# Kernel optimization log

Measured on AMD Instinct MI355X. Metric: run time of the kernel, lower is better.

The kernel has to match this reference:

```python
import jax, jax.numpy as jnp
import numpy as np

NUM_CLASSES = 10
GAMMA = 1.0
EPS = 1e-12


def setup_inputs() -> dict:
    key = jax.random.key(0)
    k1, k2, k3, k4 = jax.random.split(key, 4)
    x = jax.random.normal(k1, (1024, 64), dtype=jnp.float32)
    exemplars = jax.random.normal(k2, (50000, 64), dtype=jnp.float32)
    exemplar_labels = jax.random.randint(k3, (50000,), 0, NUM_CLASSES)
    # beta_raw initialized as softplus^{-1}(init_beta) with init_beta=1.0
    init_beta = 1.0
    beta_raw = jnp.array([np.log(np.exp(init_beta) - 1.0)], dtype=jnp.float32)
    return {"x": x, "exemplars": exemplars, "exemplar_labels": exemplar_labels,
            "beta_raw": beta_raw}


def reference(x, exemplars, exemplar_labels, beta_raw):
    # Squared Euclidean distances (weight_diag == ones) via GEMM expansion:
    # d2[b, e] = ||x_b||^2 + ||e_e||^2 - 2 <x_b, e_e>
    x2 = jnp.sum(x * x, axis=-1, keepdims=True)            # (B, 1)
    e2 = jnp.sum(exemplars * exemplars, axis=-1)           # (Ne,)
    d2 = x2 + e2[None, :] - 2.0 * (x @ exemplars.T)        # (B, Ne)
    d2 = jnp.maximum(d2, 0.0)  # true sq-dist is nonneg; guards GEMM round-off
    beta = jax.nn.softplus(beta_raw[0])
    sims = jnp.exp(-beta * d2)                              # (B, Ne)
    # scatter-add similarities into per-class bins: (C, B) -> (B, C)
    class_sims = jax.ops.segment_sum(sims.T, exemplar_labels,
                                     num_segments=NUM_CLASSES).T
    logits = GAMMA * jnp.log(class_sims + EPS)
    return logits
```

## Files before the change

kernel.cpp:

```cpp
#include <hip/hip_runtime.h>


#define NB      1024
#define NE      50000
#define NE_PAD  50176
#define KD      64
#define NC      10
#define SROWS   64
#define NSTAGE  8
#define LROW    72

using half8   = __attribute__((ext_vector_type(8))) _Float16;
using half4v  = __attribute__((ext_vector_type(4))) _Float16;
using floatx4 = __attribute__((ext_vector_type(4))) float;

__device__ __forceinline__ float softplus_f(float x) {
  return (x > 20.f) ? x : log1pf(__expf(x));
}

__global__ __launch_bounds__(256) void prep_kernel(
    const float* __restrict__ x, const float* __restrict__ ex,
    const int* __restrict__ labels, const float* __restrict__ beta_raw,
    _Float16* __restrict__ ex_h, float* __restrict__ ce,
    _Float16* __restrict__ x_h, float* __restrict__ cb,
    float* __restrict__ class_sims, int* __restrict__ lab_pad)
{
  const int tid = threadIdx.x;
  const int gid = blockIdx.x * 256 + tid;
  if (gid < NB * NC) class_sims[gid] = 0.f;

  const float beta = softplus_f(beta_raw[0]);

  const int row = blockIdx.x * 16 + (tid >> 4);
  const int l16 = tid & 15;

  if (row < NE_PAD) {
    float4 v = make_float4(0.f, 0.f, 0.f, 0.f);
    if (row < NE) v = ((const float4*)ex)[row * 16 + l16];
    half4v hv = { (_Float16)v.x, (_Float16)v.y, (_Float16)v.z, (_Float16)v.w };
    *(half4v*)(ex_h + (size_t)row * KD + l16 * 4) = hv;
    float s = v.x*v.x + v.y*v.y + v.z*v.z + v.w*v.w;
    #pragma unroll
    for (int m = 1; m < 16; m <<= 1) s += __shfl_xor(s, m, 64);
    if (l16 == 0) ce[row] = (row < NE) ? (-beta * s) : -1e30f;
    if (l16 == 1) lab_pad[row] = (row < NE) ? labels[row] : 0;
  } else {
    const int rx = row - NE_PAD;
    float4 v = ((const float4*)x)[rx * 16 + l16];
    half4v hv = { (_Float16)v.x, (_Float16)v.y, (_Float16)v.z, (_Float16)v.w };
    *(half4v*)(x_h + (size_t)rx * KD + l16 * 4) = hv;
    float s = v.x*v.x + v.y*v.y + v.z*v.z + v.w*v.w;
    #pragma unroll
    for (int m = 1; m < 16; m <<= 1) s += __shfl_xor(s, m, 64);
    if (l16 == 0) cb[rx] = -beta * s;
  }
}

__global__ __launch_bounds__(256) void main_kernel(
    const _Float16* __restrict__ ex_h, const float* __restrict__ ce,
    const _Float16* __restrict__ x_h, const float* __restrict__ cb,
    const int* __restrict__ lab_pad, const float* __restrict__ beta_raw,
    float* __restrict__ class_sims)
{
  __shared__ _Float16 Ah[2][SROWS * LROW];
  __shared__ float    Ce[2][SROWS];
  __shared__ int      Lb[2][SROWS];

  const int tid  = threadIdx.x;
  const int wave = tid >> 6;
  const int lane = tid & 63;
  const int l15  = lane & 15;
  const int quad = lane >> 4;

  const int btile = blockIdx.x;
  const int chunk = blockIdx.y;
  const int e0    = chunk * 512;
  const int bm    = btile * 64 + wave * 16;

  const float beta = softplus_f(beta_raw[0]);
  const float s2 = 2.f * beta;

  const half8* xrow = (const half8*)(x_h + (size_t)(bm + l15) * KD);
  const half8 bx0 = xrow[quad];
  const half8 bx1 = xrow[quad + 4];
  const float cbl = cb[bm + l15];

  const int srow = tid >> 2;
  const int scol = tid & 3;
  const _Float16* gsrc = ex_h + (size_t)(e0 + srow) * KD + scol * 16;
  const int lofs = srow * LROW + scol * 16;

  half8 pr0 = *(const half8*)(gsrc);
  half8 pr1 = *(const half8*)(gsrc + 8);
  float prc = 0.f; int prl = 0;
  if (wave == 0) prc = ce[e0 + lane];
  if (wave == 1) prl = lab_pad[e0 + lane];

  *(half8*)(&Ah[0][lofs])     = pr0;
  *(half8*)(&Ah[0][lofs + 8]) = pr1;
  if (wave == 0) Ce[0][lane] = prc;
  if (wave == 1) Lb[0][lane] = prl;
  __syncthreads();

  floatx4 acc = {0.f, 0.f, 0.f, 0.f};

  for (int st = 0; st < NSTAGE; ++st) {
    const int b = st & 1;

    if (st + 1 < NSTAGE) {
      const _Float16* g = gsrc + (size_t)(st + 1) * SROWS * KD;
      pr0 = *(const half8*)(g);
      pr1 = *(const half8*)(g + 8);
      if (wave == 0) prc = ce[e0 + (st + 1) * SROWS + lane];
      if (wave == 1) prl = lab_pad[e0 + (st + 1) * SROWS + lane];
    }

    #pragma unroll
    for (int sub = 0; sub < 4; ++sub) {
      const int abase = (sub * 16 + l15) * LROW + quad * 8;
      const half8 ae0 = *(const half8*)(&Ah[b][abase]);
      const half8 ae1 = *(const half8*)(&Ah[b][abase + 32]);
      const float4 ce4 = *(const float4*)(&Ce[b][sub * 16 + quad * 4]);
      const int4   lb4 = *(const int4*)(&Lb[b][sub * 16 + quad * 4]);

      floatx4 d = {0.f, 0.f, 0.f, 0.f};
      d = __builtin_amdgcn_mfma_f32_16x16x32_f16(ae0, bx0, d, 0, 0, 0);
      d = __builtin_amdgcn_mfma_f32_16x16x32_f16(ae1, bx1, d, 0, 0, 0);

      const float cef[4] = { ce4.x, ce4.y, ce4.z, ce4.w };
      half4v p;
      #pragma unroll
      for (int r = 0; r < 4; ++r) {
        const float t = fminf(fmaf(s2, d[r], cbl + cef[r]), 0.f);
        p[r] = (_Float16)__expf(t);
      }

      half4v oh;
      oh[0] = (lb4.x == l15) ? (_Float16)1.f : (_Float16)0.f;
      oh[1] = (lb4.y == l15) ? (_Float16)1.f : (_Float16)0.f;
      oh[2] = (lb4.z == l15) ? (_Float16)1.f : (_Float16)0.f;
      oh[3] = (lb4.w == l15) ? (_Float16)1.f : (_Float16)0.f;

      acc = __builtin_amdgcn_mfma_f32_16x16x16f16(oh, p, acc, 0, 0, 0);
    }

    if (st + 1 < NSTAGE) {
      __syncthreads();
      const int nb = (st + 1) & 1;
      *(half8*)(&Ah[nb][lofs])     = pr0;
      *(half8*)(&Ah[nb][lofs + 8]) = pr1;
      if (wave == 0) Ce[nb][lane] = prc;
      if (wave == 1) Lb[nb][lane] = prl;
      __syncthreads();
    }
  }

  #pragma unroll
  for (int r = 0; r < 4; ++r) {
    const int c = quad * 4 + r;
    if (c < NC) {
      __hip_atomic_fetch_add(&class_sims[(size_t)(bm + l15) * NC + c], acc[r],
                             __ATOMIC_RELAXED, __HIP_MEMORY_SCOPE_AGENT);
    }
  }
}

__global__ __launch_bounds__(256) void log_kernel(
    const float* __restrict__ cs, float* __restrict__ out)
{
  const int i = blockIdx.x * 256 + threadIdx.x;
  if (i < NB * NC) out[i] = __logf(cs[i] + 1e-12f);
}

extern "C" void kernel_launch(void* const* d_in, const int* in_sizes, int n_in,
                              void* d_out, int out_size, void* d_ws, size_t ws_size,
                              hipStream_t stream)
{
  const float* x        = (const float*)d_in[0];
  const float* ex       = (const float*)d_in[1];
  const int*   labels   = (const int*)d_in[2];
  const float* beta_raw = (const float*)d_in[3];
  float* out = (float*)d_out;

  char* ws = (char*)d_ws;
  _Float16* ex_h       = (_Float16*)ws;
  float*    ce         = (float*)(ws + 6422528);
  _Float16* x_h        = (_Float16*)(ws + 6623232);
  float*    cb         = (float*)(ws + 6754304);
  float*    class_sims = (float*)(ws + 6758400);
  int*      lab_pad    = (int*)(ws + 6799360);

  prep_kernel<<<3200, 256, 0, stream>>>(x, ex, labels, beta_raw,
                                        ex_h, ce, x_h, cb, class_sims, lab_pad);
  dim3 g(16, 98);
  main_kernel<<<g, 256, 0, stream>>>(ex_h, ce, x_h, cb, lab_pad, beta_raw, class_sims);
  log_kernel<<<40, 256, 0, stream>>>(class_sims, out);
}
```

Baseline: 102.6 us.

## Prefetch two stages ahead, drop a barrier, and remap blocks per XCD

Global loads now run two stages ahead in double register buffers, and one of the two __syncthreads per stage is removed. Exemplar chunks are padded to 104 so the grid becomes 1664 blocks, which is a multiple of 8. Block ids are remapped so that all btiles sharing a chunk land on the same XCD, improving L2 reuse of the exemplar chunk. The extra buffers cost more registers, and removing the barrier relies on the prefetch distance to keep shared-memory reuse safe.

```diff
diff --git a/kernel.cpp b/kernel.cpp
--- a/kernel.cpp
+++ b/kernel.cpp
@@ -3,7 +3,8 @@
 
 #define NB      1024
 #define NE      50000
-#define NE_PAD  50176
+#define NCHUNK  104
+#define NE_PAD  (NCHUNK * 512)
 #define KD      64
 #define NC      10
 #define SROWS   64
@@ -72,8 +73,11 @@
   const int l15  = lane & 15;
   const int quad = lane >> 4;
 
-  const int btile = blockIdx.x;
-  const int chunk = blockIdx.y;
+  const int id    = blockIdx.x;
+  const int xcd   = id & 7;
+  const int j     = id >> 3;
+  const int chunk = xcd + 8 * (j % 13);
+  const int btile = j / 13;
   const int e0    = chunk * 512;
   const int bm    = btile * 64 + wave * 16;
 
@@ -90,29 +94,37 @@
   const _Float16* gsrc = ex_h + (size_t)(e0 + srow) * KD + scol * 16;
   const int lofs = srow * LROW + scol * 16;
 
-  half8 pr0 = *(const half8*)(gsrc);
-  half8 pr1 = *(const half8*)(gsrc + 8);
-  float prc = 0.f; int prl = 0;
-  if (wave == 0) prc = ce[e0 + lane];
-  if (wave == 1) prl = lab_pad[e0 + lane];
-
-  *(half8*)(&Ah[0][lofs])     = pr0;
-  *(half8*)(&Ah[0][lofs + 8]) = pr1;
-  if (wave == 0) Ce[0][lane] = prc;
-  if (wave == 1) Lb[0][lane] = prl;
+  half8 pa[2], pb[2];
+  float pc[2] = {0.f, 0.f};
+  int   pl[2] = {0, 0};
+
+  pa[0] = *(const half8*)(gsrc);
+  pb[0] = *(const half8*)(gsrc + 8);
+  if (wave == 0) pc[0] = ce[e0 + lane];
+  if (wave == 1) pl[0] = lab_pad[e0 + lane];
+  pa[1] = *(const half8*)(gsrc + SROWS * KD);
+  pb[1] = *(const half8*)(gsrc + SROWS * KD + 8);
+  if (wave == 0) pc[1] = ce[e0 + SROWS + lane];
+  if (wave == 1) pl[1] = lab_pad[e0 + SROWS + lane];
+
+  *(half8*)(&Ah[0][lofs])     = pa[0];
+  *(half8*)(&Ah[0][lofs + 8]) = pb[0];
+  if (wave == 0) Ce[0][lane] = pc[0];
+  if (wave == 1) Lb[0][lane] = pl[0];
   __syncthreads();
 
   floatx4 acc = {0.f, 0.f, 0.f, 0.f};
 
+  #pragma unroll
   for (int st = 0; st < NSTAGE; ++st) {
     const int b = st & 1;
 
-    if (st + 1 < NSTAGE) {
-      const _Float16* g = gsrc + (size_t)(st + 1) * SROWS * KD;
-      pr0 = *(const half8*)(g);
-      pr1 = *(const half8*)(g + 8);
-      if (wave == 0) prc = ce[e0 + (st + 1) * SROWS + lane];
-      if (wave == 1) prl = lab_pad[e0 + (st + 1) * SROWS + lane];
+    if (st + 2 < NSTAGE) {
+      const _Float16* g = gsrc + (size_t)(st + 2) * SROWS * KD;
+      pa[b] = *(const half8*)(g);
+      pb[b] = *(const half8*)(g + 8);
+      if (wave == 0) pc[b] = ce[e0 + (st + 2) * SROWS + lane];
+      if (wave == 1) pl[b] = lab_pad[e0 + (st + 2) * SROWS + lane];
     }
 
     #pragma unroll
@@ -145,12 +157,11 @@
     }
 
     if (st + 1 < NSTAGE) {
-      __syncthreads();
       const int nb = (st + 1) & 1;
-      *(half8*)(&Ah[nb][lofs])     = pr0;
-      *(half8*)(&Ah[nb][lofs + 8]) = pr1;
-      if (wave == 0) Ce[nb][lane] = prc;
-      if (wave == 1) Lb[nb][lane] = prl;
+      *(half8*)(&Ah[nb][lofs])     = pa[nb];
+      *(half8*)(&Ah[nb][lofs + 8]) = pb[nb];
+      if (wave == 0) Ce[nb][lane] = pc[nb];
+      if (wave == 1) Lb[nb][lane] = pl[nb];
       __syncthreads();
     }
   }
@@ -184,15 +195,15 @@
 
   char* ws = (char*)d_ws;
   _Float16* ex_h       = (_Float16*)ws;
-  float*    ce         = (float*)(ws + 6422528);
-  _Float16* x_h        = (_Float16*)(ws + 6623232);
-  float*    cb         = (float*)(ws + 6754304);
-  float*    class_sims = (float*)(ws + 6758400);
-  int*      lab_pad    = (int*)(ws + 6799360);
-
-  prep_kernel<<<3200, 256, 0, stream>>>(x, ex, labels, beta_raw,
+  float*    ce         = (float*)(ws + 6815744);
+  _Float16* x_h        = (_Float16*)(ws + 7028736);
+  float*    cb         = (float*)(ws + 7159808);
+  float*    class_sims = (float*)(ws + 7163904);
+  int*      lab_pad    = (int*)(ws + 7204864);
+
+  prep_kernel<<<3392, 256, 0, stream>>>(x, ex, labels, beta_raw,
                                         ex_h, ce, x_h, cb, class_sims, lab_pad);
-  dim3 g(16, 98);
-  main_kernel<<<g, 256, 0, stream>>>(ex_h, ce, x_h, cb, lab_pad, beta_raw, class_sims);
+  main_kernel<<<1664, 256, 0, stream>>>(ex_h, ce, x_h, cb, lab_pad, beta_raw,
+                                        class_sims);
   log_kernel<<<40, 256, 0, stream>>>(class_sims, out);
 }
```

Measured after the change: 105.7 us. 1.03x slower.
